# Kernel tuning notes

Hardware: AMD Instinct MI355X
Metric: run time of the kernel (lower is better)

## Reference

```python
import jax, jax.numpy as jnp
import numpy as np

HID = 512
ALPHA = 0.01
PI = np.float32(np.pi)


def _mlp(x, W0, b0, W1, b1, W2, b2, W3, b3):
    # x: [..., 2] -> scalar field u(x): [...]
    h = jnp.tanh(x @ W0 + b0)
    h = jnp.tanh(h @ W1 + b1)
    h = jnp.tanh(h @ W2 + b2)
    return (h @ W3 + b3)[..., 0]


def _forcing(x):
    # f = -Delta u for u = sin(pi x) sin(pi y^2)
    xx, yy = x[:, 0], x[:, 1]
    return (-PI ** 2 * (1 + 4 * yy ** 2) * jnp.sin(PI * xx) * jnp.sin(PI * yy ** 2)
            + 2 * PI * jnp.sin(PI * xx) * jnp.cos(PI * yy ** 2))


def setup_inputs() -> dict:
    key = jax.random.key(0)
    ks = jax.random.split(key, 6)
    n_i, n_b = 20000, 800
    x_interior = jax.random.uniform(ks[0], (n_i, 2), dtype=jnp.float32)  # domain (0,1)
    theta = jnp.linspace(0.0, 2.0 * np.pi, n_b)
    x_boundary = jnp.stack([(jnp.cos(theta) + 1.0) * 0.5,
                            (jnp.sin(theta) + 1.0) * 0.5], axis=1).astype(jnp.float32)

    def w(k, shape, fan_in):
        return (jax.random.normal(k, shape, jnp.float32) / np.float32(np.sqrt(fan_in)))

    W0 = w(ks[1], (2, HID), 2)
    b0 = jnp.zeros((HID,), jnp.float32)
    W1 = w(ks[2], (HID, HID), HID)
    b1 = jnp.zeros((HID,), jnp.float32)
    W2 = w(ks[3], (HID, HID), HID)
    b2 = jnp.zeros((HID,), jnp.float32)
    W3 = w(ks[4], (HID, 1), HID)
    b3 = jnp.zeros((1,), jnp.float32)
    return dict(x_interior=x_interior, x_boundary=x_boundary,
                W0=W0, b0=b0, W1=W1, b1=b1, W2=W2, b2=b2, W3=W3, b3=b3)


def reference(x_interior, x_boundary, W0, b0, W1, b1, W2, b2, W3, b3):
    params = (W0, b0, W1, b1, W2, b2, W3, b3)

    def u_scalar(x):  # x: [2] -> scalar
        return _mlp(x, *params)

    g = jax.grad(u_scalar)

    def lap_one(x):
        # Laplacian = trace of Hessian via forward-over-reverse HVPs
        lap = jnp.float32(0.0)
        for i in range(2):
            e = jnp.zeros((2,), x.dtype).at[i].set(1.0)
            _, hv = jax.jvp(g, (x,), (e,))
            lap = lap + hv[i]
        return lap

    laplacian = jax.vmap(lap_one)(x_interior)  # [n_interior]
    interior_loss = jnp.mean((laplacian - _forcing(x_interior)) ** 2)
    boundary_loss = jnp.mean(_mlp(x_boundary, *params) ** 2)
    total_loss = ALPHA * interior_loss + boundary_loss
    return total_loss, interior_loss, boundary_loss
```

## Files before the change

### kernel.cpp

```cpp
#include <hip/hip_runtime.h>
#include <math.h>

#define HID 512
#define PPB 16
#define SLAB 512

typedef __attribute__((ext_vector_type(8))) _Float16 half8;
typedef __attribute__((ext_vector_type(4))) _Float16 half4;
typedef __attribute__((ext_vector_type(4))) float f32x4;

static __device__ __forceinline__ float fast_tanh(float x) {
    float e = __expf(2.f * x);
    return 1.f - 2.f / (e + 1.f);
}


__global__ __launch_bounds__(256) void prep_wt(
    const float* __restrict__ W1, const float* __restrict__ W2,
    _Float16* __restrict__ W1h, _Float16* __restrict__ W2h,
    unsigned* __restrict__ counter)
{
    if (blockIdx.x == 0 && threadIdx.x == 0) *counter = 0u;
    __shared__ float T[64][65];
    int b = blockIdx.x;
    const float* W = (b < 64) ? W1 : W2;
    _Float16* Wh   = (b < 64) ? W1h : W2h;
    int tb = b & 63;
    int jbG = tb >> 3, kbG = tb & 7;
    int j0 = jbG * 64, k0 = kbG * 64;
    int t = threadIdx.x;
    #pragma unroll
    for (int r = 0; r < 16; ++r) {
        int kl = r * 4 + (t >> 6);
        int jl = t & 63;
        T[kl][jl] = W[(size_t)(k0 + kl) * HID + j0 + jl];
    }
    __syncthreads();
    int ljb = t >> 6;
    int l15 = (t >> 2) & 15;
    int quad = t & 3;
    #pragma unroll
    for (int lkb = 0; lkb < 2; ++lkb) {
        half8 v;
        #pragma unroll
        for (int k8 = 0; k8 < 8; ++k8)
            v[k8] = (_Float16)T[lkb * 32 + quad * 8 + k8][ljb * 16 + l15];
        size_t out = (size_t)((jbG * 4 + ljb) * 16 + (kbG * 2 + lkb)) * SLAB
                   + (quad * 16 + l15) * 8;
        *(half8*)(Wh + out) = v;
    }
}

template<bool FULL>
static __device__ __forceinline__ void layer_pass(
    const _Float16* __restrict__ Wh, const float* __restrict__ bias,
    _Float16* Als, int wv, int lane)
{
    const int l15 = lane & 15, quad = lane >> 4;
    const int jb0 = wv * 4;
    const int loff = lane * 8;

    f32x4 acc[4][4];
    #pragma unroll
    for (int s = 0; s < 4; ++s)
        #pragma unroll
        for (int jt = 0; jt < 4; ++jt) acc[s][jt] = (f32x4)0.f;

    half8 wA[4], wB[4];
    #pragma unroll
    for (int jt = 0; jt < 4; ++jt)
        wA[jt] = *(const half8*)(Wh + (size_t)((jb0 + jt) * 16) * SLAB + loff);

    auto iter = [&](int kb, half8 (&wc)[4], half8 (&wn)[4]) {
        if (kb < 15) {
            #pragma unroll
            for (int jt = 0; jt < 4; ++jt)
                wn[jt] = *(const half8*)(Wh + (size_t)((jb0 + jt) * 16 + kb + 1) * SLAB + loff);
        }
        half8 a[4];
        #pragma unroll
        for (int s = 0; s < 4; ++s)
            a[s] = *(const half8*)(Als + (s * 16 + kb) * SLAB + loff);
        #pragma unroll
        for (int s = 0; s < 4; ++s)
            #pragma unroll
            for (int jt = 0; jt < 4; ++jt)
                acc[s][jt] = __builtin_amdgcn_mfma_f32_16x16x32_f16(
                    wc[jt], a[s], acc[s][jt], 0, 0, 0);
    };

    #pragma unroll
    for (int kb = 0; kb < 16; kb += 2) {
        iter(kb,     wA, wB);
        iter(kb + 1, wB, wA);
    }

    __syncthreads();

    #pragma unroll
    for (int jt = 0; jt < 4; ++jt) {
        const int jbase = wv * 64 + jt * 16 + quad * 4;
        const int kbp = wv * 2 + (jt >> 1);
        const int qo = (jt & 1) * 2 + (quad >> 1);
        const int e0 = (quad & 1) * 4;
        f32x4 bv = *(const f32x4*)&bias[jbase];
        half4 vh, vt1, vt2, vS;
        #pragma unroll
        for (int r = 0; r < 4; ++r) {
            float a  = fast_tanh(acc[0][jt][r] + bv[r]);
            float g  = 1.f - a * a;
            float z1 = acc[1][jt][r];
            float z2 = acc[2][jt][r];
            vh[r] = (_Float16)a;
            if (FULL) {
                vt1[r] = (_Float16)(g * z1);
                vt2[r] = (_Float16)(g * z2);
            }
            vS[r] = (_Float16)(g * acc[3][jt][r] - 2.f * a * g * (z1 * z1 + z2 * z2));
        }
        const int ooff = (qo * 16 + l15) * 8 + e0;
        *(half4*)(Als + (0 * 16 + kbp) * SLAB + ooff) = vh;
        if (FULL) {
            *(half4*)(Als + (1 * 16 + kbp) * SLAB + ooff) = vt1;
            *(half4*)(Als + (2 * 16 + kbp) * SLAB + ooff) = vt2;
        }
        *(half4*)(Als + (3 * 16 + kbp) * SLAB + ooff) = vS;
    }
    __syncthreads();
}

__global__ __launch_bounds__(512, 4) void pois_fused(
    const float* __restrict__ x_int, const float* __restrict__ x_bnd,
    const float* __restrict__ W0, const float* __restrict__ b0,
    const _Float16* __restrict__ W1h, const float* __restrict__ b1,
    const _Float16* __restrict__ W2h, const float* __restrict__ b2,
    const float* __restrict__ W3, const float* __restrict__ b3,
    float* __restrict__ partials, unsigned* __restrict__ counter,
    float* __restrict__ out, int NI, int NT, int nblk)
{
    __shared__ _Float16 Als[4 * 16 * SLAB];
    __shared__ float scU[8][16], scL[8][16], sc[32];
    __shared__ float ri[4], rb[4];
    __shared__ int lastFlag;

    const int tid = threadIdx.x;
    const int wv = tid >> 6, lane = tid & 63;
    const int l15 = lane & 15, quad = lane >> 4;
    const int p0 = blockIdx.x * PPB;

    {
        int gp = p0 + l15;
        int gpc = (gp >= NT) ? 0 : gp;
        float xx, yy;
        if (gpc < NI) { xx = x_int[2 * gpc];        yy = x_int[2 * gpc + 1]; }
        else          { xx = x_bnd[2 * (gpc - NI)]; yy = x_bnd[2 * (gpc - NI) + 1]; }
        #pragma unroll
        for (int t = 0; t < 2; ++t) {
            const int kb = wv * 2 + t;
            const int k = kb * 32 + quad * 8;
            f32x4 w0a = *(const f32x4*)&W0[k],       w0b = *(const f32x4*)&W0[k + 4];
            f32x4 w1a = *(const f32x4*)&W0[HID + k], w1b = *(const f32x4*)&W0[HID + k + 4];
            f32x4 b0a = *(const f32x4*)&b0[k],       b0b = *(const f32x4*)&b0[k + 4];
            half8 vh, vt1, vt2, vS;
            #pragma unroll
            for (int e = 0; e < 8; ++e) {
                float w0i = (e < 4) ? w0a[e] : w0b[e - 4];
                float w1i = (e < 4) ? w1a[e] : w1b[e - 4];
                float bbi = (e < 4) ? b0a[e] : b0b[e - 4];
                float a = fast_tanh(xx * w0i + yy * w1i + bbi);
                float g = 1.f - a * a;
                vh[e]  = (_Float16)a;
                vt1[e] = (_Float16)(g * w0i);
                vt2[e] = (_Float16)(g * w1i);
                vS[e]  = (_Float16)(-2.f * a * g * (w0i * w0i + w1i * w1i));
            }
            const int off = lane * 8;
            *(half8*)(Als + (0 * 16 + kb) * SLAB + off) = vh;
            *(half8*)(Als + (1 * 16 + kb) * SLAB + off) = vt1;
            *(half8*)(Als + (2 * 16 + kb) * SLAB + off) = vt2;
            *(half8*)(Als + (3 * 16 + kb) * SLAB + off) = vS;
        }
    }
    __syncthreads();

    layer_pass<true >(W1h, b1, Als, wv, lane);
    layer_pass<false>(W2h, b2, Als, wv, lane);

    {
        float u = 0.f, lap = 0.f;
        #pragma unroll
        for (int t = 0; t < 2; ++t) {
            const int kb = wv * 2 + t;
            const int k = kb * 32 + quad * 8;
            f32x4 wa = *(const f32x4*)&W3[k], wb = *(const f32x4*)&W3[k + 4];
            half8 hh = *(const half8*)(Als + (0 * 16 + kb) * SLAB + lane * 8);
            half8 ss = *(const half8*)(Als + (3 * 16 + kb) * SLAB + lane * 8);
            #pragma unroll
            for (int e = 0; e < 4; ++e) {
                u   += (float)hh[e] * wa[e] + (float)hh[e + 4] * wb[e];
                lap += (float)ss[e] * wa[e] + (float)ss[e + 4] * wb[e];
            }
        }
        u   += __shfl_xor(u, 16);   u   += __shfl_xor(u, 32);
        lap += __shfl_xor(lap, 16); lap += __shfl_xor(lap, 32);
        if (lane < 16) { scU[wv][l15] = u; scL[wv][l15] = lap; }
    }
    __syncthreads();

    if (tid < 16) {
        const int p = tid;
        float u = 0.f, lap = 0.f;
        #pragma unroll
        for (int w = 0; w < 8; ++w) { u += scU[w][p]; lap += scL[w][p]; }
        int gp = p0 + p;
        float vi = 0.f, vb = 0.f;
        if (gp < NI) {
            const float PIf = 3.14159265358979323846f;
            float xx = x_int[2 * gp], yy = x_int[2 * gp + 1];
            float sx = sinf(PIf * xx);
            float y2 = yy * yy;
            float sy = sinf(PIf * y2), cy = cosf(PIf * y2);
            float f = -PIf * PIf * (1.f + 4.f * y2) * sx * sy + 2.f * PIf * sx * cy;
            float r = lap - f;
            vi = r * r;
        } else if (gp < NT) {
            float uu = u + b3[0];
            vb = uu * uu;
        }
        sc[p * 2] = vi; sc[p * 2 + 1] = vb;
    }
    __syncthreads();
    if (tid == 0) {
        float svi = 0.f, svb = 0.f;
        #pragma unroll
        for (int p = 0; p < PPB; ++p) { svi += sc[p * 2]; svb += sc[p * 2 + 1]; }
        partials[blockIdx.x] = svi;
        partials[nblk + blockIdx.x] = svb;
        __threadfence();
        unsigned old = atomicAdd(counter, 1u);
        lastFlag = (old == (unsigned)(nblk - 1));
    }
    __syncthreads();

    if (lastFlag) {
        __threadfence();
        if (tid < 256) {
            float si = 0.f, sb = 0.f;
            for (int i = tid; i < nblk; i += 256) {
                si += partials[i];
                sb += partials[nblk + i];
            }
            #pragma unroll
            for (int off = 32; off > 0; off >>= 1) {
                si += __shfl_xor(si, off);
                sb += __shfl_xor(sb, off);
            }
            int w = tid >> 6;
            if ((tid & 63) == 0) { ri[w] = si; rb[w] = sb; }
        }
    }
    __syncthreads();
    if (lastFlag && tid == 0) {
        float inter = (ri[0] + ri[1] + ri[2] + ri[3]) / (float)NI;
        float bound = (rb[0] + rb[1] + rb[2] + rb[3]) / (float)(NT - NI);
        out[0] = 0.01f * inter + bound;
        out[1] = inter;
        out[2] = bound;
    }
}

extern "C" void kernel_launch(void* const* d_in, const int* in_sizes, int n_in,
                              void* d_out, int out_size, void* d_ws, size_t ws_size,
                              hipStream_t stream)
{
    const float* x_int = (const float*)d_in[0];
    const float* x_bnd = (const float*)d_in[1];
    const float* W0 = (const float*)d_in[2];
    const float* b0 = (const float*)d_in[3];
    const float* W1 = (const float*)d_in[4];
    const float* b1 = (const float*)d_in[5];
    const float* W2 = (const float*)d_in[6];
    const float* b2 = (const float*)d_in[7];
    const float* W3 = (const float*)d_in[8];
    const float* b3 = (const float*)d_in[9];

    int NI = in_sizes[0] / 2;
    int NB = in_sizes[1] / 2;
    int NT = NI + NB;
    int nblk = (NT + PPB - 1) / PPB;
    (void)NB;

    float* partials = (float*)d_ws;
    unsigned* counter = (unsigned*)((char*)d_ws + 12288);
    _Float16* W1h = (_Float16*)((char*)d_ws + 16384);
    _Float16* W2h = W1h + 262144;

    prep_wt<<<128, 256, 0, stream>>>(W1, W2, W1h, W2h, counter);

    pois_fused<<<nblk, 512, 0, stream>>>(
        x_int, x_bnd, W0, b0, W1h, b1, W2h, b2, W3, b3,
        partials, counter, (float*)d_out, NI, NT, nblk);
}
```

Measured before the change: 207.4 us.

## Switch to 32x32x16 MFMA tiles with 32 points per block and 1024 threads

Replaces the 16x16x32 MFMA tiling with 32x32x16 MFMA instructions. The prepacked fp16 weight layout and the LDS activation layout are reworked to match. Each block now processes 32 points with 16 waves, each wave owning 32 output neurons, so every weight fragment loaded from global memory is reused across more points. The trade-offs are a larger LDS footprint (128 KB per block), different register pressure, and fewer blocks resident per CU.

```diff
diff --git a/kernel.cpp b/kernel.cpp
--- a/kernel.cpp
+++ b/kernel.cpp
@@ -2,18 +2,17 @@
 #include <math.h>
 
 #define HID 512
-#define PPB 16
-#define SLAB 512
-
-typedef __attribute__((ext_vector_type(8))) _Float16 half8;
-typedef __attribute__((ext_vector_type(4))) _Float16 half4;
-typedef __attribute__((ext_vector_type(4))) float f32x4;
+#define PPB 32
+
+typedef __attribute__((ext_vector_type(8)))  _Float16 half8;
+typedef __attribute__((ext_vector_type(4)))  _Float16 half4;
+typedef __attribute__((ext_vector_type(4)))  float f32x4;
+typedef __attribute__((ext_vector_type(16))) float f32x16;
 
 static __device__ __forceinline__ float fast_tanh(float x) {
     float e = __expf(2.f * x);
     return 1.f - 2.f / (e + 1.f);
 }
-
 
 __global__ __launch_bounds__(256) void prep_wt(
     const float* __restrict__ W1, const float* __restrict__ W2,
@@ -36,17 +35,19 @@
         T[kl][jl] = W[(size_t)(k0 + kl) * HID + j0 + jl];
     }
     __syncthreads();
-    int ljb = t >> 6;
-    int l15 = (t >> 2) & 15;
-    int quad = t & 3;
+    int ol  = t & 63;
+    int og  = t >> 6;
+    int jb_l  = og >> 1;
+    int ks_hi = og & 1;
     #pragma unroll
     for (int lkb = 0; lkb < 2; ++lkb) {
+        int kstep_l = ks_hi * 2 + lkb;
         half8 v;
         #pragma unroll
-        for (int k8 = 0; k8 < 8; ++k8)
-            v[k8] = (_Float16)T[lkb * 32 + quad * 8 + k8][ljb * 16 + l15];
-        size_t out = (size_t)((jbG * 4 + ljb) * 16 + (kbG * 2 + lkb)) * SLAB
-                   + (quad * 16 + l15) * 8;
+        for (int e = 0; e < 8; ++e)
+            v[e] = (_Float16)T[kstep_l * 16 + (ol >> 5) * 8 + e][jb_l * 32 + (ol & 31)];
+        size_t out = (size_t)((jbG * 2 + jb_l) * 32 + kbG * 4 + kstep_l) * 512
+                   + ol * 8;
         *(half8*)(Wh + out) = v;
     }
 }
@@ -56,80 +57,72 @@
     const _Float16* __restrict__ Wh, const float* __restrict__ bias,
     _Float16* Als, int wv, int lane)
 {
-    const int l15 = lane & 15, quad = lane >> 4;
-    const int jb0 = wv * 4;
     const int loff = lane * 8;
-
-    f32x4 acc[4][4];
+    const _Float16* Wp = Wh + (size_t)wv * 32 * 512;
+
+    f32x16 acc[4];
+    #pragma unroll
+    for (int s = 0; s < 4; ++s) acc[s] = (f32x16)0.f;
+
+    half8 wf0 = *(const half8*)(Wp + 0 * 512 + loff);
+    half8 wf1 = *(const half8*)(Wp + 1 * 512 + loff);
+    half8 a[4];
     #pragma unroll
     for (int s = 0; s < 4; ++s)
-        #pragma unroll
-        for (int jt = 0; jt < 4; ++jt) acc[s][jt] = (f32x4)0.f;
-
-    half8 wA[4], wB[4];
-    #pragma unroll
-    for (int jt = 0; jt < 4; ++jt)
-        wA[jt] = *(const half8*)(Wh + (size_t)((jb0 + jt) * 16) * SLAB + loff);
-
-    auto iter = [&](int kb, half8 (&wc)[4], half8 (&wn)[4]) {
-        if (kb < 15) {
-            #pragma unroll
-            for (int jt = 0; jt < 4; ++jt)
-                wn[jt] = *(const half8*)(Wh + (size_t)((jb0 + jt) * 16 + kb + 1) * SLAB + loff);
-        }
-        half8 a[4];
-        #pragma unroll
-        for (int s = 0; s < 4; ++s)
-            a[s] = *(const half8*)(Als + (s * 16 + kb) * SLAB + loff);
-        #pragma unroll
-        for (int s = 0; s < 4; ++s)
-            #pragma unroll
-            for (int jt = 0; jt < 4; ++jt)
-                acc[s][jt] = __builtin_amdgcn_mfma_f32_16x16x32_f16(
-                    wc[jt], a[s], acc[s][jt], 0, 0, 0);
+        a[s] = *(const half8*)(Als + (s * 32 + 0) * 512 + loff);
+
+    auto step = [&](int i, half8& wreg) {
+        #pragma unroll
+        for (int s = 0; s < 4; ++s) {
+            acc[s] = __builtin_amdgcn_mfma_f32_32x32x16_f16(wreg, a[s], acc[s], 0, 0, 0);
+            if (i < 31)
+                a[s] = *(const half8*)(Als + (s * 32 + i + 1) * 512 + loff);
+        }
+        if (i < 30)
+            wreg = *(const half8*)(Wp + (size_t)(i + 2) * 512 + loff);
     };
 
     #pragma unroll
-    for (int kb = 0; kb < 16; kb += 2) {
-        iter(kb,     wA, wB);
-        iter(kb + 1, wB, wA);
-    }
-
-    __syncthreads();
-
-    #pragma unroll
-    for (int jt = 0; jt < 4; ++jt) {
-        const int jbase = wv * 64 + jt * 16 + quad * 4;
-        const int kbp = wv * 2 + (jt >> 1);
-        const int qo = (jt & 1) * 2 + (quad >> 1);
-        const int e0 = (quad & 1) * 4;
-        f32x4 bv = *(const f32x4*)&bias[jbase];
+    for (int i = 0; i < 32; i += 2) {
+        step(i,     wf0);
+        step(i + 1, wf1);
+    }
+
+    __syncthreads();
+
+    const int p  = lane & 31;
+    const int hi = lane >> 5;
+    #pragma unroll
+    for (int g = 0; g < 4; ++g) {
+        const int jv  = wv * 32 + 8 * g + 4 * hi;
+        const int kst = wv * 2 + (g >> 1);
+        f32x4 bv = *(const f32x4*)&bias[jv];
         half4 vh, vt1, vt2, vS;
         #pragma unroll
-        for (int r = 0; r < 4; ++r) {
-            float a  = fast_tanh(acc[0][jt][r] + bv[r]);
-            float g  = 1.f - a * a;
-            float z1 = acc[1][jt][r];
-            float z2 = acc[2][jt][r];
-            vh[r] = (_Float16)a;
+        for (int m = 0; m < 4; ++m) {
+            float a_ = fast_tanh(acc[0][g * 4 + m] + bv[m]);
+            float gg = 1.f - a_ * a_;
+            float z1 = acc[1][g * 4 + m];
+            float z2 = acc[2][g * 4 + m];
+            vh[m] = (_Float16)a_;
             if (FULL) {
-                vt1[r] = (_Float16)(g * z1);
-                vt2[r] = (_Float16)(g * z2);
-            }
-            vS[r] = (_Float16)(g * acc[3][jt][r] - 2.f * a * g * (z1 * z1 + z2 * z2));
-        }
-        const int ooff = (qo * 16 + l15) * 8 + e0;
-        *(half4*)(Als + (0 * 16 + kbp) * SLAB + ooff) = vh;
+                vt1[m] = (_Float16)(gg * z1);
+                vt2[m] = (_Float16)(gg * z2);
+            }
+            vS[m] = (_Float16)(gg * acc[3][g * 4 + m] - 2.f * a_ * gg * (z1 * z1 + z2 * z2));
+        }
+        const int ooff = ((g & 1) * 32 + p) * 8 + 4 * hi;
+        *(half4*)(Als + (0 * 32 + kst) * 512 + ooff) = vh;
         if (FULL) {
-            *(half4*)(Als + (1 * 16 + kbp) * SLAB + ooff) = vt1;
-            *(half4*)(Als + (2 * 16 + kbp) * SLAB + ooff) = vt2;
-        }
-        *(half4*)(Als + (3 * 16 + kbp) * SLAB + ooff) = vS;
-    }
-    __syncthreads();
-}
-
-__global__ __launch_bounds__(512, 4) void pois_fused(
+            *(half4*)(Als + (1 * 32 + kst) * 512 + ooff) = vt1;
+            *(half4*)(Als + (2 * 32 + kst) * 512 + ooff) = vt2;
+        }
+        *(half4*)(Als + (3 * 32 + kst) * 512 + ooff) = vS;
+    }
+    __syncthreads();
+}
+
+__global__ __launch_bounds__(1024, 4) void pois_fused(
     const float* __restrict__ x_int, const float* __restrict__ x_bnd,
     const float* __restrict__ W0, const float* __restrict__ b0,
     const _Float16* __restrict__ W1h, const float* __restrict__ b1,
@@ -138,26 +131,27 @@
     float* __restrict__ partials, unsigned* __restrict__ counter,
     float* __restrict__ out, int NI, int NT, int nblk)
 {
-    __shared__ _Float16 Als[4 * 16 * SLAB];
-    __shared__ float scU[8][16], scL[8][16], sc[32];
+    __shared__ _Float16 Als[4 * 32 * 512];
+    __shared__ float scU[16][32], scL[16][32], sc[64];
     __shared__ float ri[4], rb[4];
     __shared__ int lastFlag;
 
     const int tid = threadIdx.x;
     const int wv = tid >> 6, lane = tid & 63;
-    const int l15 = lane & 15, quad = lane >> 4;
+    const int p  = lane & 31;
+    const int hi = lane >> 5;
     const int p0 = blockIdx.x * PPB;
 
     {
-        int gp = p0 + l15;
+        int gp = p0 + p;
         int gpc = (gp >= NT) ? 0 : gp;
         float xx, yy;
         if (gpc < NI) { xx = x_int[2 * gpc];        yy = x_int[2 * gpc + 1]; }
         else          { xx = x_bnd[2 * (gpc - NI)]; yy = x_bnd[2 * (gpc - NI) + 1]; }
         #pragma unroll
         for (int t = 0; t < 2; ++t) {
-            const int kb = wv * 2 + t;
-            const int k = kb * 32 + quad * 8;
+            const int kstep = wv * 2 + t;
+            const int k = kstep * 16 + hi * 8;
             f32x4 w0a = *(const f32x4*)&W0[k],       w0b = *(const f32x4*)&W0[k + 4];
             f32x4 w1a = *(const f32x4*)&W0[HID + k], w1b = *(const f32x4*)&W0[HID + k + 4];
             f32x4 b0a = *(const f32x4*)&b0[k],       b0b = *(const f32x4*)&b0[k + 4];
@@ -175,10 +169,10 @@
                 vS[e]  = (_Float16)(-2.f * a * g * (w0i * w0i + w1i * w1i));
             }
             const int off = lane * 8;
-            *(half8*)(Als + (0 * 16 + kb) * SLAB + off) = vh;
-            *(half8*)(Als + (1 * 16 + kb) * SLAB + off) = vt1;
-            *(half8*)(Als + (2 * 16 + kb) * SLAB + off) = vt2;
-            *(half8*)(Als + (3 * 16 + kb) * SLAB + off) = vS;
+            *(half8*)(Als + (0 * 32 + kstep) * 512 + off) = vh;
+            *(half8*)(Als + (1 * 32 + kstep) * 512 + off) = vt1;
+            *(half8*)(Als + (2 * 32 + kstep) * 512 + off) = vt2;
+            *(half8*)(Als + (3 * 32 + kstep) * 512 + off) = vS;
         }
     }
     __syncthreads();
@@ -190,29 +184,29 @@
         float u = 0.f, lap = 0.f;
         #pragma unroll
         for (int t = 0; t < 2; ++t) {
-            const int kb = wv * 2 + t;
-            const int k = kb * 32 + quad * 8;
+            const int kstep = wv * 2 + t;
+            const int k = kstep * 16 + hi * 8;
             f32x4 wa = *(const f32x4*)&W3[k], wb = *(const f32x4*)&W3[k + 4];
-            half8 hh = *(const half8*)(Als + (0 * 16 + kb) * SLAB + lane * 8);
-            half8 ss = *(const half8*)(Als + (3 * 16 + kb) * SLAB + lane * 8);
+            half8 hh = *(const half8*)(Als + (0 * 32 + kstep) * 512 + lane * 8);
+            half8 ss = *(const half8*)(Als + (3 * 32 + kstep) * 512 + lane * 8);
             #pragma unroll
             for (int e = 0; e < 4; ++e) {
                 u   += (float)hh[e] * wa[e] + (float)hh[e + 4] * wb[e];
                 lap += (float)ss[e] * wa[e] + (float)ss[e + 4] * wb[e];
             }
         }
-        u   += __shfl_xor(u, 16);   u   += __shfl_xor(u, 32);
-        lap += __shfl_xor(lap, 16); lap += __shfl_xor(lap, 32);
-        if (lane < 16) { scU[wv][l15] = u; scL[wv][l15] = lap; }
-    }
-    __syncthreads();
-
-    if (tid < 16) {
-        const int p = tid;
+        u   += __shfl_xor(u, 32);
+        lap += __shfl_xor(lap, 32);
+        if (lane < 32) { scU[wv][p] = u; scL[wv][p] = lap; }
+    }
+    __syncthreads();
+
+    if (tid < 32) {
+        const int pp = tid;
         float u = 0.f, lap = 0.f;
         #pragma unroll
-        for (int w = 0; w < 8; ++w) { u += scU[w][p]; lap += scL[w][p]; }
-        int gp = p0 + p;
+        for (int w = 0; w < 16; ++w) { u += scU[w][pp]; lap += scL[w][pp]; }
+        int gp = p0 + pp;
         float vi = 0.f, vb = 0.f;
         if (gp < NI) {
             const float PIf = 3.14159265358979323846f;
@@ -227,13 +221,13 @@
             float uu = u + b3[0];
             vb = uu * uu;
         }
-        sc[p * 2] = vi; sc[p * 2 + 1] = vb;
+        sc[pp * 2] = vi; sc[pp * 2 + 1] = vb;
     }
     __syncthreads();
     if (tid == 0) {
         float svi = 0.f, svb = 0.f;
         #pragma unroll
-        for (int p = 0; p < PPB; ++p) { svi += sc[p * 2]; svb += sc[p * 2 + 1]; }
+        for (int pp = 0; pp < PPB; ++pp) { svi += sc[pp * 2]; svb += sc[pp * 2 + 1]; }
         partials[blockIdx.x] = svi;
         partials[nblk + blockIdx.x] = svb;
         __threadfence();
@@ -297,7 +291,7 @@
 
     prep_wt<<<128, 256, 0, stream>>>(W1, W2, W1h, W2h, counter);
 
-    pois_fused<<<nblk, 512, 0, stream>>>(
+    pois_fused<<<nblk, 1024, 0, stream>>>(
         x_int, x_bnd, W0, b0, W1h, b1, W2h, b2, W3, b3,
         partials, counter, (float*)d_out, NI, NT, nblk);
 }
```

New measurement: 211.3 us. Within noise of the previous version (+1.9%).
